# Kernel optimization log

Measured on AMD Instinct MI355X. Metric: run time of the kernel, lower is better.

## Reference

```python
import jax, jax.numpy as jnp
import numpy as np

N_NODES = 50000
N_EDGES = 1600000
IN_FEATS = 256
NUM_HEADS = 4
OUT_FEATS = 32
NEG_SLOPE = 0.2


def setup_inputs() -> dict:
    key = jax.random.key(0)
    k_feat, k_src, k_dst, k_w, k_al, k_ar = jax.random.split(key, 6)
    feat = jax.random.normal(k_feat, (N_NODES, IN_FEATS), dtype=jnp.float32)
    src = jax.random.randint(k_src, (N_EDGES,), 0, N_NODES, dtype=jnp.int32)
    dst = jax.random.randint(k_dst, (N_EDGES,), 0, N_NODES, dtype=jnp.int32)
    # Glorot/xavier-like scales
    w_scale = np.sqrt(2.0 / (IN_FEATS + NUM_HEADS * OUT_FEATS)).astype(np.float32)
    a_scale = np.sqrt(2.0 / (1 + OUT_FEATS)).astype(np.float32)
    W_fc = jax.random.normal(k_w, (NUM_HEADS * OUT_FEATS, IN_FEATS), dtype=jnp.float32) * w_scale
    attn_l = jax.random.normal(k_al, (1, NUM_HEADS, OUT_FEATS), dtype=jnp.float32) * a_scale
    attn_r = jax.random.normal(k_ar, (1, NUM_HEADS, OUT_FEATS), dtype=jnp.float32) * a_scale
    bias = jnp.zeros((NUM_HEADS * OUT_FEATS,), dtype=jnp.float32)
    return {"feat": feat, "W_fc": W_fc, "attn_l": attn_l, "attn_r": attn_r,
            "bias": bias, "src": src, "dst": dst}


def reference(feat, W_fc, attn_l, attn_r, bias, src, dst):
    N = feat.shape[0]
    H, F = NUM_HEADS, OUT_FEATS
    # dense projection: [N, H, F]
    h = (feat @ W_fc.T).reshape(N, H, F)
    # per-node attention logits: [N, H]
    el = (h * attn_l).sum(axis=-1)
    er = (h * attn_r).sum(axis=-1)
    # u_add_v edge score + leaky relu: [E, H]
    e = el[src] + er[dst]
    e = jnp.where(e >= 0, e, NEG_SLOPE * e)
    # segment softmax over destination nodes
    m = jax.ops.segment_max(e, dst, num_segments=N)          # [N, H]
    m = jnp.where(jnp.isfinite(m), m, 0.0)                   # guard 0-in-degree
    e_exp = jnp.exp(e - m[dst])                              # [E, H]
    denom = jax.ops.segment_sum(e_exp, dst, num_segments=N)  # [N, H]
    denom = jnp.where(denom > 0, denom, 1.0)
    a = e_exp / denom[dst]                                   # [E, H]
    # weighted message aggregation: [N, H, F]
    msg = h[src] * a[:, :, None]                             # [E, H, F]
    out = jax.ops.segment_sum(msg, dst, num_segments=N)
    out = out + bias.reshape(1, H, F)
    return out
```

## Files before the change

kernel.cpp:

```cpp
#include <hip/hip_runtime.h>

typedef __attribute__((ext_vector_type(8))) short bf16x8;
typedef __attribute__((ext_vector_type(4))) float f32x4;

#define IN_F 256
#define HF 128
#define NHEADS 4
#define NEG 0.2f

#define RB 256
#define NBP 200
#define CHUNK 6400
#define ITPT 25
#define BCAP 10000

#define PART_SMEM ((256 * 3 + CHUNK) * 4)

__device__ __forceinline__ unsigned short f2bf(float x) {
    unsigned u = __float_as_uint(x);
    unsigned r = (u + 0x7FFFu + ((u >> 16) & 1u)) >> 16;
    return (unsigned short)r;
}
__device__ __forceinline__ float bf2f(unsigned short b) {
    return __uint_as_float((unsigned)b << 16);
}
__device__ __forceinline__ bf16x8 cvt8(float4 x, float4 y) {
    bf16x8 r;
    r[0] = f2bf(x.x); r[1] = f2bf(x.y); r[2] = f2bf(x.z); r[3] = f2bf(x.w);
    r[4] = f2bf(y.x); r[5] = f2bf(y.y); r[6] = f2bf(y.z); r[7] = f2bf(y.w);
    return r;
}

__global__ __launch_bounds__(256) void wconv_kernel(const float* __restrict__ W,
                                                    unsigned short* __restrict__ Wb) {
    int i = (blockIdx.x * 256 + threadIdx.x) * 4;
    if (i < HF * IN_F) {
        float4 v = *(const float4*)&W[i];
        ushort4 o;
        o.x = f2bf(v.x); o.y = f2bf(v.y); o.z = f2bf(v.z); o.w = f2bf(v.w);
        *(ushort4*)&Wb[i] = o;
    }
}

__global__ __launch_bounds__(256) void fused1_kernel(
    const float* __restrict__ feat, const unsigned short* __restrict__ Wb,
    const float* __restrict__ al, const float* __restrict__ ar,
    unsigned short* __restrict__ hb, float* __restrict__ el, float* __restrict__ er,
    const int* __restrict__ src, const int* __restrict__ dst,
    int* __restrict__ ebuf, int* __restrict__ cntArr, int* __restrict__ ofsArr,
    int N, int E, int GG)
{
    extern __shared__ char smem[];
    const int t = threadIdx.x;

    if ((int)blockIdx.x < GG) {
        const int lane = t & 63;
        const int wid = t >> 6;
        const int base = blockIdx.x * 128 + wid * 32;
        const int lr = lane & 15;
        const int lkO = (lane >> 4) * 8;

        const int r0 = base + lr;
        const int r1 = base + 16 + lr;
        const bool v0 = r0 < N, v1 = r1 < N;
        const float* arow0 = feat + (size_t)r0 * IN_F + lkO;
        const float* arow1 = feat + (size_t)r1 * IN_F + lkO;

        f32x4 acc[2][8];
#pragma unroll
        for (int mi = 0; mi < 2; mi++)
#pragma unroll
            for (int ni = 0; ni < 8; ni++) acc[mi][ni] = (f32x4){0.f, 0.f, 0.f, 0.f};

        const float4 z4 = make_float4(0.f, 0.f, 0.f, 0.f);
#pragma unroll
        for (int ks = 0; ks < 8; ks++) {
            const int k0 = ks * 32;
            bf16x8 a0, a1;
            {
                float4 x0 = v0 ? *(const float4*)(arow0 + k0) : z4;
                float4 x1 = v0 ? *(const float4*)(arow0 + k0 + 4) : z4;
                a0 = cvt8(x0, x1);
                float4 y0 = v1 ? *(const float4*)(arow1 + k0) : z4;
                float4 y1 = v1 ? *(const float4*)(arow1 + k0 + 4) : z4;
                a1 = cvt8(y0, y1);
            }
            bf16x8 b[8];
#pragma unroll
            for (int ni = 0; ni < 8; ni++)
                b[ni] = *(const bf16x8*)&Wb[(size_t)(ni * 16 + lr) * IN_F + k0 + lkO];
#pragma unroll
            for (int ni = 0; ni < 8; ni++) {
                acc[0][ni] = __builtin_amdgcn_mfma_f32_16x16x32_bf16(a0, b[ni], acc[0][ni], 0, 0, 0);
                acc[1][ni] = __builtin_amdgcn_mfma_f32_16x16x32_bf16(a1, b[ni], acc[1][ni], 0, 0, 0);
            }
        }

        float al_c[8], ar_c[8];
#pragma unroll
        for (int ni = 0; ni < 8; ni++) {
            al_c[ni] = al[ni * 16 + lr];
            ar_c[ni] = ar[ni * 16 + lr];
        }
        const int crow = (lane >> 4) * 4;
#pragma unroll
        for (int mi = 0; mi < 2; mi++)
#pragma unroll
            for (int j = 0; j < 4; j++) {
                int n = base + mi * 16 + crow + j;
                if (n < N) {
#pragma unroll
                    for (int ni = 0; ni < 8; ni++)
                        hb[(size_t)n * HF + ni * 16 + lr] = f2bf(acc[mi][ni][j]);
                }
                float e[4], r[4];
#pragma unroll
                for (int h = 0; h < 4; h++) {
                    e[h] = acc[mi][2 * h][j] * al_c[2 * h] + acc[mi][2 * h + 1][j] * al_c[2 * h + 1];
                    r[h] = acc[mi][2 * h][j] * ar_c[2 * h] + acc[mi][2 * h + 1][j] * ar_c[2 * h + 1];
                }
#pragma unroll
                for (int off = 1; off < 16; off <<= 1) {
#pragma unroll
                    for (int h = 0; h < 4; h++) {
                        e[h] += __shfl_xor(e[h], off);
                        r[h] += __shfl_xor(r[h], off);
                    }
                }
                if (lr == 0 && n < N) {
                    *(float4*)&el[(size_t)n * 4] = make_float4(e[0], e[1], e[2], e[3]);
                    *(float4*)&er[(size_t)n * 4] = make_float4(r[0], r[1], r[2], r[3]);
                }
            }
    } else {
        int* cnt = (int*)smem;
        int* sc  = cnt + 256;
        int* cur = sc + 256;
        int* stage = cur + 256;
        const int blk = blockIdx.x - GG;
        const int eb = blk * CHUNK;
        cnt[t] = 0;
        __syncthreads();

        int bkt[ITPT], ent[ITPT];
#pragma unroll
        for (int i = 0; i < ITPT; i++) {
            int idx = eb + i * 256 + t;
            int b = NBP - 1, e = 0;
            if (idx < E) {
                int d = dst[idx];
                int s = src[idx];
                b = d >> 8;
                e = s | ((d & 255) << 24);
            }
            bkt[i] = b;
            ent[i] = e;
            atomicAdd(&cnt[b], 1);
        }
        __syncthreads();
        int orig = cnt[t];
        sc[t] = orig;
        __syncthreads();
        for (int off = 1; off < 256; off <<= 1) {
            int v = (t >= off) ? sc[t - off] : 0;
            __syncthreads();
            sc[t] += v;
            __syncthreads();
        }
        int excl = sc[t] - orig;
        if (t < NBP) {
            cntArr[blk * NBP + t] = orig;
            ofsArr[blk * NBP + t] = excl;
        }
        cur[t] = excl;
        __syncthreads();
#pragma unroll
        for (int i = 0; i < ITPT; i++) {
            int pos = atomicAdd(&cur[bkt[i]], 1);
            stage[pos] = ent[i];
        }
        __syncthreads();
#pragma unroll
        for (int i = 0; i < ITPT; i++) {
            int idx = i * 256 + t;
            ebuf[eb + idx] = stage[idx];
        }
    }
}

__global__ __launch_bounds__(256) void bscan_kernel(const int* __restrict__ cntArr,
                                                    int* __restrict__ bucketStart, int nblk) {
    __shared__ int sums[256];
    const int t = threadIdx.x;
    int s = 0;
    if (t < NBP)
        for (int blk = 0; blk < nblk; blk++) s += cntArr[blk * NBP + t];
    sums[t] = s;
    __syncthreads();
    for (int off = 1; off < 256; off <<= 1) {
        int v = (t >= off) ? sums[t - off] : 0;
        __syncthreads();
        sums[t] += v;
        __syncthreads();
    }
    if (t < NBP) bucketStart[t] = sums[t] - s;
}

__global__ __launch_bounds__(256) void bsort_kernel(const int* __restrict__ ebuf,
                                                    const int* __restrict__ cntArr,
                                                    const int* __restrict__ ofsArr,
                                                    const int* __restrict__ bucketStart,
                                                    int* __restrict__ rowStart,
                                                    int* __restrict__ esrc,
                                                    int nblk, int N, int E) {
    __shared__ int lcnt[256];
    __shared__ int lsc[256];
    __shared__ int lcur[256];
    __shared__ int sorted[BCAP];
    const int b = blockIdx.x, t = threadIdx.x;
    const int gbase = bucketStart[b];
    lcnt[t] = 0;
    __syncthreads();

    int rbase = 0, rlen = 0;
    if (t < nblk) {
        rbase = t * CHUNK + ofsArr[t * NBP + b];
        rlen = cntArr[t * NBP + b];
    }
    int i = 0;
    for (; i + 3 < rlen; i += 4) {
        unsigned e0 = (unsigned)ebuf[rbase + i];
        unsigned e1 = (unsigned)ebuf[rbase + i + 1];
        unsigned e2 = (unsigned)ebuf[rbase + i + 2];
        unsigned e3 = (unsigned)ebuf[rbase + i + 3];
        atomicAdd(&lcnt[e0 >> 24], 1);
        atomicAdd(&lcnt[e1 >> 24], 1);
        atomicAdd(&lcnt[e2 >> 24], 1);
        atomicAdd(&lcnt[e3 >> 24], 1);
    }
    for (; i < rlen; i++) {
        unsigned e = (unsigned)ebuf[rbase + i];
        atomicAdd(&lcnt[e >> 24], 1);
    }
    __syncthreads();
    int orig = lcnt[t];
    lsc[t] = orig;
    __syncthreads();
    for (int off = 1; off < 256; off <<= 1) {
        int v = (t >= off) ? lsc[t - off] : 0;
        __syncthreads();
        lsc[t] += v;
        __syncthreads();
    }
    int excl = lsc[t] - orig;
    int node = b * RB + t;
    if (node < N) rowStart[node] = gbase + excl;
    if (b == 0 && t == 0) rowStart[N] = E;
    lcur[t] = excl;
    __syncthreads();
    i = 0;
    for (; i + 3 < rlen; i += 4) {
        unsigned e0 = (unsigned)ebuf[rbase + i];
        unsigned e1 = (unsigned)ebuf[rbase + i + 1];
        unsigned e2 = (unsigned)ebuf[rbase + i + 2];
        unsigned e3 = (unsigned)ebuf[rbase + i + 3];
        sorted[atomicAdd(&lcur[e0 >> 24], 1)] = (int)(e0 & 0xFFFFFFu);
        sorted[atomicAdd(&lcur[e1 >> 24], 1)] = (int)(e1 & 0xFFFFFFu);
        sorted[atomicAdd(&lcur[e2 >> 24], 1)] = (int)(e2 & 0xFFFFFFu);
        sorted[atomicAdd(&lcur[e3 >> 24], 1)] = (int)(e3 & 0xFFFFFFu);
    }
    for (; i < rlen; i++) {
        unsigned e = (unsigned)ebuf[rbase + i];
        sorted[atomicAdd(&lcur[e >> 24], 1)] = (int)(e & 0xFFFFFFu);
    }
    __syncthreads();
    const int total = lsc[255];
    for (int k = t; k < total; k += 256) esrc[gbase + k] = sorted[k];
}

__global__ __launch_bounds__(256) void agg_kernel(const int* __restrict__ rowStart,
                                                  const int* __restrict__ esrc,
                                                  const unsigned short* __restrict__ hb,
                                                  const float* __restrict__ el,
                                                  const float* __restrict__ er,
                                                  const float* __restrict__ bias,
                                                  float* __restrict__ out, int N) {
    const int wid = threadIdx.x >> 6;
    const int lane = threadIdx.x & 63;
    const int n = blockIdx.x * 4 + wid;
    if (n >= N) return;
    const int lg = lane & 15;
    const int grp = lane >> 4;
    const int head = lg >> 2;
    const float ern = er[n * NHEADS + head];
    const int beg = rowStart[n];
    const int end = rowStart[n + 1];

    float acc[8];
#pragma unroll
    for (int i = 0; i < 8; i++) acc[i] = 0.f;
    float den = 0.f;

#pragma unroll 2
    for (int j = beg + grp; j < end; j += 4) {
        int s = esrc[j];
        float x = el[s * NHEADS + head] + ern;
        x = x >= 0.f ? x : NEG * x;
        float sv = __expf(x);
        uint4 hv = *(const uint4*)&hb[(size_t)s * HF + lg * 8];
        acc[0] += sv * bf2f((unsigned short)(hv.x & 0xFFFFu));
        acc[1] += sv * bf2f((unsigned short)(hv.x >> 16));
        acc[2] += sv * bf2f((unsigned short)(hv.y & 0xFFFFu));
        acc[3] += sv * bf2f((unsigned short)(hv.y >> 16));
        acc[4] += sv * bf2f((unsigned short)(hv.z & 0xFFFFu));
        acc[5] += sv * bf2f((unsigned short)(hv.z >> 16));
        acc[6] += sv * bf2f((unsigned short)(hv.w & 0xFFFFu));
        acc[7] += sv * bf2f((unsigned short)(hv.w >> 16));
        den += sv;
    }

#pragma unroll
    for (int off = 16; off < 64; off <<= 1) {
#pragma unroll
        for (int i = 0; i < 8; i++) acc[i] += __shfl_xor(acc[i], off);
        den += __shfl_xor(den, off);
    }

    if (lane < 16) {
        float inv = 1.f / (den > 0.f ? den : 1.f);
        float4 b0 = *(const float4*)&bias[lg * 8];
        float4 b1 = *(const float4*)&bias[lg * 8 + 4];
        float4 o0, o1;
        o0.x = acc[0] * inv + b0.x; o0.y = acc[1] * inv + b0.y;
        o0.z = acc[2] * inv + b0.z; o0.w = acc[3] * inv + b0.w;
        o1.x = acc[4] * inv + b1.x; o1.y = acc[5] * inv + b1.y;
        o1.z = acc[6] * inv + b1.z; o1.w = acc[7] * inv + b1.w;
        *(float4*)&out[(size_t)n * HF + lg * 8] = o0;
        *(float4*)&out[(size_t)n * HF + lg * 8 + 4] = o1;
    }
}

extern "C" void kernel_launch(void* const* d_in, const int* in_sizes, int n_in,
                              void* d_out, int out_size, void* d_ws, size_t ws_size,
                              hipStream_t stream) {
    const float* feat = (const float*)d_in[0];
    const float* W    = (const float*)d_in[1];
    const float* al   = (const float*)d_in[2];
    const float* ar   = (const float*)d_in[3];
    const float* bias = (const float*)d_in[4];
    const int*   src  = (const int*)d_in[5];
    const int*   dst  = (const int*)d_in[6];
    const int N = in_sizes[0] / IN_F;
    const int E = in_sizes[5];
    float* out = (float*)d_out;

    const int nblk = (E + CHUNK - 1) / CHUNK;
    const int NBUCK = (N + RB - 1) / RB;
    const int GG = (N + 127) / 128;

    unsigned short* hb = (unsigned short*)d_ws;
    unsigned short* Wb = hb + (size_t)N * HF;
    float* el       = (float*)(Wb + HF * IN_F);
    float* er       = el + (size_t)N * NHEADS;
    int* rowStart   = (int*)(er + (size_t)N * NHEADS);
    int* esrc       = rowStart + (N + 1);
    int* ebuf       = esrc + E;
    int* cntArr     = ebuf + (size_t)nblk * CHUNK;
    int* ofsArr     = cntArr + (size_t)nblk * NBP;
    int* bucketStart= ofsArr + (size_t)nblk * NBP;

    wconv_kernel<<<(HF * IN_F / 4 + 255) / 256, 256, 0, stream>>>(W, Wb);
    fused1_kernel<<<GG + nblk, 256, PART_SMEM, stream>>>(
        feat, Wb, al, ar, hb, el, er, src, dst, ebuf, cntArr, ofsArr, N, E, GG);
    bscan_kernel<<<1, 256, 0, stream>>>(cntArr, bucketStart, nblk);
    bsort_kernel<<<NBUCK, 256, 0, stream>>>(ebuf, cntArr, ofsArr, bucketStart,
                                            rowStart, esrc, nblk, N, E);
    agg_kernel<<<(N + 3) / 4, 256, 0, stream>>>(rowStart, esrc, hb, el, er, bias, out, N);
}
```

Measured before the change: 163.8 us.

## Split fused GEMM/partition kernel and drop LDS staging in edge partition

Splits the combined GEMM-plus-edge-partition kernel into two separate launches. The GEMM now handles 16 rows per wave instead of 32, which halves accumulator registers and doubles the block count. The partition kernel records each edge's atomic rank during counting and scatters directly to global memory, removing the 25.6KB LDS staging buffer and the second atomic pass. The cost is an extra kernel launch, the loss of overlap between GEMM and partition blocks, and less W reuse per wave.

```diff
diff --git a/kernel.cpp b/kernel.cpp
--- a/kernel.cpp
+++ b/kernel.cpp
@@ -13,8 +13,6 @@
 #define CHUNK 6400
 #define ITPT 25
 #define BCAP 10000
-
-#define PART_SMEM ((256 * 3 + CHUNK) * 4)
 
 __device__ __forceinline__ unsigned short f2bf(float x) {
     unsigned u = __float_as_uint(x);
@@ -42,149 +40,127 @@
     }
 }
 
-__global__ __launch_bounds__(256) void fused1_kernel(
+__global__ __launch_bounds__(256) void gemm_kernel(
     const float* __restrict__ feat, const unsigned short* __restrict__ Wb,
     const float* __restrict__ al, const float* __restrict__ ar,
     unsigned short* __restrict__ hb, float* __restrict__ el, float* __restrict__ er,
-    const int* __restrict__ src, const int* __restrict__ dst,
-    int* __restrict__ ebuf, int* __restrict__ cntArr, int* __restrict__ ofsArr,
-    int N, int E, int GG)
+    int N)
 {
-    extern __shared__ char smem[];
     const int t = threadIdx.x;
-
-    if ((int)blockIdx.x < GG) {
-        const int lane = t & 63;
-        const int wid = t >> 6;
-        const int base = blockIdx.x * 128 + wid * 32;
-        const int lr = lane & 15;
-        const int lkO = (lane >> 4) * 8;
-
-        const int r0 = base + lr;
-        const int r1 = base + 16 + lr;
-        const bool v0 = r0 < N, v1 = r1 < N;
-        const float* arow0 = feat + (size_t)r0 * IN_F + lkO;
-        const float* arow1 = feat + (size_t)r1 * IN_F + lkO;
-
-        f32x4 acc[2][8];
-#pragma unroll
-        for (int mi = 0; mi < 2; mi++)
-#pragma unroll
-            for (int ni = 0; ni < 8; ni++) acc[mi][ni] = (f32x4){0.f, 0.f, 0.f, 0.f};
-
-        const float4 z4 = make_float4(0.f, 0.f, 0.f, 0.f);
-#pragma unroll
-        for (int ks = 0; ks < 8; ks++) {
-            const int k0 = ks * 32;
-            bf16x8 a0, a1;
-            {
-                float4 x0 = v0 ? *(const float4*)(arow0 + k0) : z4;
-                float4 x1 = v0 ? *(const float4*)(arow0 + k0 + 4) : z4;
-                a0 = cvt8(x0, x1);
-                float4 y0 = v1 ? *(const float4*)(arow1 + k0) : z4;
-                float4 y1 = v1 ? *(const float4*)(arow1 + k0 + 4) : z4;
-                a1 = cvt8(y0, y1);
+    const int lane = t & 63;
+    const int wid = t >> 6;
+    const int base = blockIdx.x * 64 + wid * 16;
+    const int lr = lane & 15;
+    const int lkO = (lane >> 4) * 8;
+
+    const int r0 = base + lr;
+    const bool v0 = r0 < N;
+    const float* arow = feat + (size_t)r0 * IN_F + lkO;
+
+    f32x4 acc[8];
+#pragma unroll
+    for (int ni = 0; ni < 8; ni++) acc[ni] = (f32x4){0.f, 0.f, 0.f, 0.f};
+
+    const float4 z4 = make_float4(0.f, 0.f, 0.f, 0.f);
+#pragma unroll
+    for (int ks = 0; ks < 8; ks++) {
+        const int k0 = ks * 32;
+        float4 x0 = v0 ? *(const float4*)(arow + k0) : z4;
+        float4 x1 = v0 ? *(const float4*)(arow + k0 + 4) : z4;
+        bf16x8 a0 = cvt8(x0, x1);
+        bf16x8 b[8];
+#pragma unroll
+        for (int ni = 0; ni < 8; ni++)
+            b[ni] = *(const bf16x8*)&Wb[(size_t)(ni * 16 + lr) * IN_F + k0 + lkO];
+#pragma unroll
+        for (int ni = 0; ni < 8; ni++)
+            acc[ni] = __builtin_amdgcn_mfma_f32_16x16x32_bf16(a0, b[ni], acc[ni], 0, 0, 0);
+    }
+
+    float al_c[8], ar_c[8];
+#pragma unroll
+    for (int ni = 0; ni < 8; ni++) {
+        al_c[ni] = al[ni * 16 + lr];
+        ar_c[ni] = ar[ni * 16 + lr];
+    }
+    const int crow = (lane >> 4) * 4;
+#pragma unroll
+    for (int j = 0; j < 4; j++) {
+        int n = base + crow + j;
+        if (n < N) {
+#pragma unroll
+            for (int ni = 0; ni < 8; ni++)
+                hb[(size_t)n * HF + ni * 16 + lr] = f2bf(acc[ni][j]);
+        }
+        float e[4], r[4];
+#pragma unroll
+        for (int h = 0; h < 4; h++) {
+            e[h] = acc[2 * h][j] * al_c[2 * h] + acc[2 * h + 1][j] * al_c[2 * h + 1];
+            r[h] = acc[2 * h][j] * ar_c[2 * h] + acc[2 * h + 1][j] * ar_c[2 * h + 1];
+        }
+#pragma unroll
+        for (int off = 1; off < 16; off <<= 1) {
+#pragma unroll
+            for (int h = 0; h < 4; h++) {
+                e[h] += __shfl_xor(e[h], off);
+                r[h] += __shfl_xor(r[h], off);
             }
-            bf16x8 b[8];
-#pragma unroll
-            for (int ni = 0; ni < 8; ni++)
-                b[ni] = *(const bf16x8*)&Wb[(size_t)(ni * 16 + lr) * IN_F + k0 + lkO];
-#pragma unroll
-            for (int ni = 0; ni < 8; ni++) {
-                acc[0][ni] = __builtin_amdgcn_mfma_f32_16x16x32_bf16(a0, b[ni], acc[0][ni], 0, 0, 0);
-                acc[1][ni] = __builtin_amdgcn_mfma_f32_16x16x32_bf16(a1, b[ni], acc[1][ni], 0, 0, 0);
-            }
-        }
-
-        float al_c[8], ar_c[8];
-#pragma unroll
-        for (int ni = 0; ni < 8; ni++) {
-            al_c[ni] = al[ni * 16 + lr];
-            ar_c[ni] = ar[ni * 16 + lr];
-        }
-        const int crow = (lane >> 4) * 4;
-#pragma unroll
-        for (int mi = 0; mi < 2; mi++)
-#pragma unroll
-            for (int j = 0; j < 4; j++) {
-                int n = base + mi * 16 + crow + j;
-                if (n < N) {
-#pragma unroll
-                    for (int ni = 0; ni < 8; ni++)
-                        hb[(size_t)n * HF + ni * 16 + lr] = f2bf(acc[mi][ni][j]);
-                }
-                float e[4], r[4];
-#pragma unroll
-                for (int h = 0; h < 4; h++) {
-                    e[h] = acc[mi][2 * h][j] * al_c[2 * h] + acc[mi][2 * h + 1][j] * al_c[2 * h + 1];
-                    r[h] = acc[mi][2 * h][j] * ar_c[2 * h] + acc[mi][2 * h + 1][j] * ar_c[2 * h + 1];
-                }
-#pragma unroll
-                for (int off = 1; off < 16; off <<= 1) {
-#pragma unroll
-                    for (int h = 0; h < 4; h++) {
-                        e[h] += __shfl_xor(e[h], off);
-                        r[h] += __shfl_xor(r[h], off);
-                    }
-                }
-                if (lr == 0 && n < N) {
-                    *(float4*)&el[(size_t)n * 4] = make_float4(e[0], e[1], e[2], e[3]);
-                    *(float4*)&er[(size_t)n * 4] = make_float4(r[0], r[1], r[2], r[3]);
-                }
-            }
-    } else {
-        int* cnt = (int*)smem;
-        int* sc  = cnt + 256;
-        int* cur = sc + 256;
-        int* stage = cur + 256;
-        const int blk = blockIdx.x - GG;
-        const int eb = blk * CHUNK;
-        cnt[t] = 0;
-        __syncthreads();
-
-        int bkt[ITPT], ent[ITPT];
-#pragma unroll
-        for (int i = 0; i < ITPT; i++) {
-            int idx = eb + i * 256 + t;
-            int b = NBP - 1, e = 0;
-            if (idx < E) {
-                int d = dst[idx];
-                int s = src[idx];
-                b = d >> 8;
-                e = s | ((d & 255) << 24);
-            }
-            bkt[i] = b;
-            ent[i] = e;
-            atomicAdd(&cnt[b], 1);
-        }
-        __syncthreads();
-        int orig = cnt[t];
-        sc[t] = orig;
-        __syncthreads();
-        for (int off = 1; off < 256; off <<= 1) {
-            int v = (t >= off) ? sc[t - off] : 0;
-            __syncthreads();
-            sc[t] += v;
-            __syncthreads();
-        }
-        int excl = sc[t] - orig;
-        if (t < NBP) {
-            cntArr[blk * NBP + t] = orig;
-            ofsArr[blk * NBP + t] = excl;
-        }
-        cur[t] = excl;
-        __syncthreads();
-#pragma unroll
-        for (int i = 0; i < ITPT; i++) {
-            int pos = atomicAdd(&cur[bkt[i]], 1);
-            stage[pos] = ent[i];
-        }
-        __syncthreads();
-#pragma unroll
-        for (int i = 0; i < ITPT; i++) {
-            int idx = i * 256 + t;
-            ebuf[eb + idx] = stage[idx];
-        }
+        }
+        if (lr == 0 && n < N) {
+            *(float4*)&el[(size_t)n * 4] = make_float4(e[0], e[1], e[2], e[3]);
+            *(float4*)&er[(size_t)n * 4] = make_float4(r[0], r[1], r[2], r[3]);
+        }
+    }
+}
+
+__global__ __launch_bounds__(256) void part_kernel(const int* __restrict__ src,
+                                                   const int* __restrict__ dst,
+                                                   int* __restrict__ ebuf,
+                                                   int* __restrict__ cntArr,
+                                                   int* __restrict__ ofsArr, int E) {
+    __shared__ int cnt[256];
+    __shared__ int sc[256];
+    const int blk = blockIdx.x, t = threadIdx.x;
+    const int eb = blk * CHUNK;
+    cnt[t] = 0;
+    __syncthreads();
+
+    int bkt[ITPT], ent[ITPT], rank[ITPT];
+#pragma unroll
+    for (int i = 0; i < ITPT; i++) {
+        int idx = eb + i * 256 + t;
+        int b = NBP - 1, e = 0;
+        if (idx < E) {
+            int d = dst[idx];
+            int s = src[idx];
+            b = d >> 8;
+            e = s | ((d & 255) << 24);
+        }
+        bkt[i] = b;
+        ent[i] = e;
+        rank[i] = atomicAdd(&cnt[b], 1);
+    }
+    __syncthreads();
+    int orig = cnt[t];
+    sc[t] = orig;
+    __syncthreads();
+    for (int off = 1; off < 256; off <<= 1) {
+        int v = (t >= off) ? sc[t - off] : 0;
+        __syncthreads();
+        sc[t] += v;
+        __syncthreads();
+    }
+    int excl = sc[t] - orig;
+    if (t < NBP) {
+        cntArr[blk * NBP + t] = orig;
+        ofsArr[blk * NBP + t] = excl;
+    }
+    cnt[t] = excl;
+    __syncthreads();
+#pragma unroll
+    for (int i = 0; i < ITPT; i++) {
+        int pos = cnt[bkt[i]] + rank[i];
+        ebuf[eb + pos] = ent[i];
     }
 }
 
@@ -356,7 +332,6 @@
 
     const int nblk = (E + CHUNK - 1) / CHUNK;
     const int NBUCK = (N + RB - 1) / RB;
-    const int GG = (N + 127) / 128;
 
     unsigned short* hb = (unsigned short*)d_ws;
     unsigned short* Wb = hb + (size_t)N * HF;
@@ -370,8 +345,8 @@
     int* bucketStart= ofsArr + (size_t)nblk * NBP;
 
     wconv_kernel<<<(HF * IN_F / 4 + 255) / 256, 256, 0, stream>>>(W, Wb);
-    fused1_kernel<<<GG + nblk, 256, PART_SMEM, stream>>>(
-        feat, Wb, al, ar, hb, el, er, src, dst, ebuf, cntArr, ofsArr, N, E, GG);
+    part_kernel<<<nblk, 256, 0, stream>>>(src, dst, ebuf, cntArr, ofsArr, E);
+    gemm_kernel<<<(N + 63) / 64, 256, 0, stream>>>(feat, Wb, al, ar, hb, el, er, N);
     bscan_kernel<<<1, 256, 0, stream>>>(cntArr, bucketStart, nblk);
     bsort_kernel<<<NBUCK, 256, 0, stream>>>(ebuf, cntArr, ofsArr, bucketStart,
                                             rowStart, esrc, nblk, N, E);
```

New measurement: 192.8 us. 1.18x slower.
